# Optimization experiments

Measured on AMD Instinct MI355X. Metric: run time of the kernel, lower is better.

Reference implementation:

```python
import jax, jax.numpy as jnp
import numpy as np

B, T, D, H, E, S, K = 2, 2048, 768, 1536, 8, 1, 2
STD = 0.02


def setup_inputs() -> dict:
    key = jax.random.key(0)
    ks = jax.random.split(key, 8)
    x = jax.random.normal(ks[0], (B, T, D), jnp.float32)
    router_w = jax.random.normal(ks[1], (E, D), jnp.float32) * STD
    sw1 = jax.random.normal(ks[2], (S, D, H), jnp.float32) * STD
    sw2 = jax.random.normal(ks[3], (S, D, H), jnp.float32) * STD
    sproj = jax.random.normal(ks[4], (S, H, D), jnp.float32) * STD
    ew1 = jax.random.normal(ks[5], (E, D, H), jnp.float32) * STD
    ew2 = jax.random.normal(ks[6], (E, D, H), jnp.float32) * STD
    eproj = jax.random.normal(ks[7], (E, H, D), jnp.float32) * STD
    return {"x": x, "router_w": router_w, "sw1": sw1, "sw2": sw2,
            "sproj": sproj, "ew1": ew1, "ew2": ew2, "eproj": eproj,
            "top_k": K}


def reference(x, router_w, sw1, sw2, sproj, ew1, ew2, eproj, top_k):
    n_experts = router_w.shape[0]
    # Shared experts (SwiGLU), summed over the shared-expert axis s.
    a = jnp.einsum('btd,sdh->bsth', x, sw1)
    b = jnp.einsum('btd,sdh->bsth', x, sw2)
    shared_out = jnp.einsum('bsth,shd->btd', jax.nn.silu(a) * b, sproj)  # [B,T,D]

    # Router: note the original applies softmax and calls the result `logits`,
    # returning it as the second output.
    probs = jax.nn.softmax(jnp.einsum('btd,ed->bte', x, router_w), axis=-1)  # [B,T,E]
    top_vals, top_idx = jax.lax.top_k(probs, top_k)
    weights = top_vals / jnp.sum(top_vals, axis=-1, keepdims=True)  # renormalized [B,T,K]

    # Dense combine weights: combine[b,t,e] = sum_k weights[b,t,k] * 1[top_idx[b,t,k]==e]
    combine = jnp.sum(jax.nn.one_hot(top_idx, n_experts, dtype=x.dtype)
                      * weights[..., None], axis=-2)  # [B,T,E]

    # Routed experts: compute every expert densely, then mask/weight by combine.
    ea = jnp.einsum('btd,edh->bteh', x, ew1)
    eb = jnp.einsum('btd,edh->bteh', x, ew2)
    routed = jnp.einsum('bteh,ehd,bte->btd', jax.nn.silu(ea) * eb, eproj, combine)

    return shared_out + routed, probs
```

## Files before the change

### kernel.cpp

```cpp
#include <hip/hip_runtime.h>

typedef unsigned short u16;
typedef __bf16 bf16x8 __attribute__((ext_vector_type(8)));
typedef float f32x4 __attribute__((ext_vector_type(4)));

__device__ __forceinline__ u16 f2bf(float f) {
  union { float f; unsigned u; } v; v.f = f;
  return (u16)((v.u + 0x7fffu + ((v.u >> 16) & 1u)) >> 16);
}

#define GLDS16(g, l)                                                          \
  __builtin_amdgcn_global_load_lds(                                           \
      (const __attribute__((address_space(1))) void*)(g),                     \
      (__attribute__((address_space(3))) void*)(l), 16, 0, 0)

#define SBAR()  __builtin_amdgcn_s_barrier()
#define SCHED() __builtin_amdgcn_sched_barrier(0)
#define VMCNT(n) asm volatile("s_waitcnt vmcnt(" #n ")" ::: "memory")

#define NTOK 4096
#define DIM  768
#define HID  1536
#define NEXP 8
#define SLAB 1536
#define CAPR (NEXP * SLAB)
#define SHB  CAPR
#define NSLOT (CAPR + NTOK)
#define MAXT1 64
#define MAXT2 128
#define CSTRIDE 32

__global__ __launch_bounds__(256) void k_prep(const float* __restrict__ x,
                                              const float* __restrict__ rw,
                                              const float* __restrict__ ew1,
                                              const float* __restrict__ sw1,
                                              const float* __restrict__ ew2,
                                              const float* __restrict__ sw2,
                                              const float* __restrict__ eproj,
                                              const float* __restrict__ sproj,
                                              u16* __restrict__ dstBase,
                                              u16* __restrict__ xb,
                                              float* __restrict__ probs,
                                              int* __restrict__ cnt,
                                              int* __restrict__ slotTok,
                                              float* __restrict__ slotW,
                                              int* __restrict__ tokSlot) {
  constexpr size_t SL = (size_t)HID * DIM;
  const int z = blockIdx.z;
  if (z < 27) {
    __shared__ u16 tile[64][65];
    const float* src;
    int R, C, bxx = blockIdx.x, byy = blockIdx.y;
    if (z < 9)       { src = (z < 8) ? ew1 + (size_t)z * SL : sw1; R = DIM; C = HID; }
    else if (z < 18) { const int q = z - 9;  src = (q < 8) ? ew2 + (size_t)q * SL : sw2; R = DIM; C = HID; }
    else             { const int q = z - 18; src = (q < 8) ? eproj + (size_t)q * SL : sproj;
                       R = HID; C = DIM; const int t = bxx; bxx = byy; byy = t; }
    u16* dst = dstBase + (size_t)z * SL;
    const int c0 = bxx * 64, r0 = byy * 64;
    const int tx = threadIdx.x, ty = threadIdx.y;
    #pragma unroll
    for (int i = 0; i < 16; i++)
      tile[ty + 4 * i][tx] = f2bf(src[(size_t)(r0 + ty + 4 * i) * C + c0 + tx]);
    __syncthreads();
    #pragma unroll
    for (int i = 0; i < 16; i++)
      dst[(size_t)(c0 + ty + 4 * i) * R + r0 + tx] = tile[tx][ty + 4 * i];
    return;
  }
  __shared__ int   sI1[16], sI2[16];
  __shared__ float sW1[16], sW2[16];
  const int tid = threadIdx.y * 64 + threadIdx.x;
  const int wv = tid >> 6, lane = tid & 63;
  const int rb = blockIdx.y * 24 + blockIdx.x;
  for (int j = wv; j < 15; j += 4) {
    const int t = rb + 288 * j;
    if (t >= NTOK) continue;
    const float* xr = x + (size_t)t * DIM;
    u16* xbr = xb + (size_t)t * DIM;
    float acc[NEXP] = {0, 0, 0, 0, 0, 0, 0, 0};
    #pragma unroll
    for (int i = 0; i < DIM / 64; i++) {
      const int d = lane + 64 * i;
      const float xv = xr[d];
      xbr[d] = f2bf(xv);
      #pragma unroll
      for (int e = 0; e < NEXP; e++) acc[e] += xv * rw[e * DIM + d];
    }
    #pragma unroll
    for (int e = 0; e < NEXP; e++)
      #pragma unroll
      for (int s = 32; s > 0; s >>= 1) acc[e] += __shfl_xor(acc[e], s, 64);
    if (lane == 0) {
      float mx = acc[0];
      #pragma unroll
      for (int e = 1; e < NEXP; e++) mx = fmaxf(mx, acc[e]);
      float p[NEXP], sum = 0.f;
      #pragma unroll
      for (int e = 0; e < NEXP; e++) { p[e] = expf(acc[e] - mx); sum += p[e]; }
      const float inv = 1.f / sum;
      #pragma unroll
      for (int e = 0; e < NEXP; e++) p[e] *= inv;
      #pragma unroll
      for (int e = 0; e < NEXP; e++) probs[(size_t)t * NEXP + e] = p[e];
      int i1 = 0;
      #pragma unroll
      for (int e = 1; e < NEXP; e++) if (p[e] > p[i1]) i1 = e;
      int i2 = (i1 == 0) ? 1 : 0;
      #pragma unroll
      for (int e = 0; e < NEXP; e++) if (e != i1 && p[e] > p[i2]) i2 = e;
      const float s2 = 1.f / (p[i1] + p[i2]);
      sI1[j] = i1; sI2[j] = i2;
      sW1[j] = p[i1] * s2; sW2[j] = p[i2] * s2;
      slotTok[SHB + t] = t; slotW[SHB + t] = 1.f;
    }
  }
  __syncthreads();
  if (tid < NEXP) {
    const int e = tid;
    int c = 0;
    for (int j = 0; j < 15; j++) {
      const int t = rb + 288 * j;
      if (t < NTOK && (sI1[j] == e || sI2[j] == e)) c++;
    }
    if (c) {
      const int base = atomicAdd(&cnt[e * CSTRIDE], c);
      if (base + c <= SLAB) {
        int k = 0;
        for (int j = 0; j < 15; j++) {
          const int t = rb + 288 * j;
          if (t >= NTOK) continue;
          if (sI1[j] == e) {
            const int s = e * SLAB + base + k;
            slotTok[s] = t; slotW[s] = sW1[j]; tokSlot[2 * t] = s; k++;
          } else if (sI2[j] == e) {
            const int s = e * SLAB + base + k;
            slotTok[s] = t; slotW[s] = sW2[j]; tokSlot[2 * t + 1] = s; k++;
          }
        }
      }
    }
  }
}

__device__ __forceinline__ int decode_tile(const int* __restrict__ cnt, int bx,
                                           int rows_log2, int nShared, int* m0out) {
  int e = -1, m0 = 0, acc = 0;
  #pragma unroll
  for (int ee = 0; ee < NEXP; ee++) {
    const int tl = (cnt[ee * CSTRIDE] + ((1 << rows_log2) - 1)) >> rows_log2;
    if (bx >= acc && bx < acc + tl) { e = ee; m0 = ee * SLAB + ((bx - acc) << rows_log2); }
    acc += tl;
  }
  if (e < 0) {
    const int sx = bx - acc;
    if (sx >= 0 && sx < nShared) { e = NEXP; m0 = SHB + (sx << rows_log2); }
  }
  *m0out = m0;
  return e;
}

__global__ __launch_bounds__(512, 2) void k_gemm1(const u16* __restrict__ xb,
                                                  const u16* __restrict__ w1t,
                                                  const u16* __restrict__ w2t,
                                                  const int* __restrict__ cnt,
                                                  const int* __restrict__ slotTok,
                                                  const float* __restrict__ slotW,
                                                  u16* __restrict__ hidden) {
  __shared__ alignas(16) u16 L[2][32768];
  const int bid = blockIdx.x;
  const int wgid = (bid & 7) * 96 + (bid >> 3);
  const int bx = wgid % MAXT1, by = wgid / MAXT1;
  int m0;
  const int e = decode_tile(cnt, bx, 8, NTOK / 256, &m0);
  if (e < 0) return;
  const int nBase = by * 128;
  constexpr size_t SL = (size_t)HID * DIM;
  const u16* w1 = w1t + (size_t)e * SL;
  const u16* w2 = w2t + (size_t)e * SL;
  const int tid = threadIdx.x, w = tid >> 6, lane = tid & 63;
  const int wr = w >> 1, wc = w & 1;

  const int srow = tid >> 2;
  const int kcol = ((tid & 3) ^ ((tid >> 3) & 3)) * 8;
  const int tokA0 = slotTok[m0 + srow];
  const int tokA1 = slotTok[m0 + 128 + srow];
  const u16* gA0 = xb + (size_t)tokA0 * DIM + kcol;
  const u16* gA1 = xb + (size_t)tokA1 * DIM + kcol;
  const u16* gB1 = w1 + (size_t)(nBase + srow) * DIM + kcol;
  const u16* gB2 = w2 + (size_t)(nBase + srow) * DIM + kcol;
  const int dA0 = tid * 8, dA1 = 4096 + tid * 8, dB = tid * 8;

  const int rl = lane & 15;
  const int kq = lane >> 4;
  const int aBase = (wr * 64 + rl) * 32 + (kq ^ ((rl >> 1) & 3)) * 8;
  const int bBase = (wc * 64 + rl) * 32 + (kq ^ ((rl >> 1) & 3)) * 8;

  f32x4 acc1[4][4], acc2[4][4];
  const f32x4 vz = {0.f, 0.f, 0.f, 0.f};
  #pragma unroll
  for (int m = 0; m < 4; m++)
    #pragma unroll
    for (int n = 0; n < 4; n++) { acc1[m][n] = vz; acc2[m][n] = vz; }

#define G1_STKH(d, koff, kh) do {                                             \
    GLDS16(gA0 + (koff), &L[d][(kh) * 8192 + dA0]);                           \
    GLDS16(gA1 + (koff), &L[d][(kh) * 8192 + dA1]);                           \
    GLDS16(gB1 + (koff), &L[d][16384 + (kh) * 4096 + dB]);                    \
    GLDS16(gB2 + (koff), &L[d][24576 + (kh) * 4096 + dB]); } while (0)

#define G1_PH(d, kh, dostage, sd, skh, koff, vm) do {                         \
    bf16x8 av[4], b1v[4], b2v[4];                                             \
    _Pragma("unroll")                                                         \
    for (int n = 0; n < 4; n++) {                                             \
      b1v[n] = *(const bf16x8*)&L[d][16384 + (kh) * 4096 + bBase + n * 512];  \
      b2v[n] = *(const bf16x8*)&L[d][24576 + (kh) * 4096 + bBase + n * 512];  \
    }                                                                         \
    _Pragma("unroll")                                                         \
    for (int m = 0; m < 4; m++)                                               \
      av[m] = *(const bf16x8*)&L[d][(kh) * 8192 + aBase + m * 512];           \
    SCHED();                                                                  \
    if (dostage) { G1_STKH(sd, koff, skh); SCHED(); }                         \
    __builtin_amdgcn_s_setprio(1);                                            \
    _Pragma("unroll")                                                         \
    for (int m = 0; m < 4; m++)                                               \
      _Pragma("unroll")                                                       \
      for (int n = 0; n < 4; n++) {                                           \
        acc1[m][n] = __builtin_amdgcn_mfma_f32_16x16x32_bf16(av[m], b1v[n], acc1[m][n], 0, 0, 0); \
        acc2[m][n] = __builtin_amdgcn_mfma_f32_16x16x32_bf16(av[m], b2v[n], acc2[m][n], 0, 0, 0); \
      }                                                                       \
    __builtin_amdgcn_s_setprio(0);                                            \
    SCHED(); VMCNT(vm); SBAR(); SCHED();                                      \
  } while (0)

  G1_STKH(0, 0, 0);
  G1_STKH(0, 32, 1);
  G1_STKH(1, 64, 0);
  SCHED(); VMCNT(8); SBAR(); SCHED();

  for (int i = 0; i < 5; i++) {
    const int kt = i * 128;
    G1_PH(0, 0, true, 1, 1, kt + 96,  8);
    G1_PH(0, 1, true, 0, 0, kt + 128, 8);
    G1_PH(1, 0, true, 0, 1, kt + 160, 8);
    G1_PH(1, 1, true, 1, 0, kt + 192, 8);
  }
  G1_PH(0, 0, true, 1, 1, 736, 8);
  G1_PH(0, 1, false, 0, 0, 0, 4);
  G1_PH(1, 0, false, 0, 0, 0, 0);
  G1_PH(1, 1, false, 0, 0, 0, 0);
#undef G1_PH
#undef G1_STKH

  #pragma unroll
  for (int m = 0; m < 4; m++)
    #pragma unroll
    for (int r = 0; r < 4; r++) {
      const int slot = m0 + wr * 64 + m * 16 + (lane >> 4) * 4 + r;
      const float cwv = slotW[slot];
      #pragma unroll
      for (int n = 0; n < 4; n++) {
        const int hcol = nBase + wc * 64 + n * 16 + (lane & 15);
        const float v1 = acc1[m][n][r], v2 = acc2[m][n][r];
        hidden[(size_t)slot * HID + hcol] = f2bf((v1 / (1.f + __expf(-v1))) * v2 * cwv);
      }
    }
}

__global__ __launch_bounds__(256, 2) void k_gemm2(const u16* __restrict__ hid,
                                                  const u16* __restrict__ pjt,
                                                  const int* __restrict__ cnt,
                                                  float* __restrict__ g2) {
  __shared__ alignas(16) u16 L[2][16384];
  const int bid = blockIdx.x;
  const int wgid = (bid & 7) * 96 + (bid >> 3);
  const int bx = wgid % MAXT2, by = wgid / MAXT2;
  int m0;
  const int e = decode_tile(cnt, bx, 7, NTOK / 128, &m0);
  if (e < 0) return;
  const int nBase = by * 128;
  constexpr size_t SL = (size_t)HID * DIM;
  const u16* pj = pjt + (size_t)e * SL;
  const int tid = threadIdx.x, w = tid >> 6, lane = tid & 63;
  const int wr = w >> 1, wc = w & 1;

  const int r0 = tid >> 2;
  const int kcol = ((tid & 3) ^ ((tid >> 3) & 3)) * 8;
  const u16* gA0 = hid + (size_t)(m0 + r0) * HID + kcol;
  const u16* gA1 = hid + (size_t)(m0 + 64 + r0) * HID + kcol;
  const u16* gB0 = pj + (size_t)(nBase + r0) * HID + kcol;
  const u16* gB1p = pj + (size_t)(nBase + 64 + r0) * HID + kcol;
  const int d0 = tid * 8, d1 = 2048 + tid * 8;

  const int rl = lane & 15;
  const int kq = lane >> 4;
  const int aBase = (wr * 64 + rl) * 32 + (kq ^ ((rl >> 1) & 3)) * 8;
  const int bBase = (wc * 64 + rl) * 32 + (kq ^ ((rl >> 1) & 3)) * 8;

  f32x4 acc[4][4];
  const f32x4 vz = {0.f, 0.f, 0.f, 0.f};
  #pragma unroll
  for (int m = 0; m < 4; m++)
    #pragma unroll
    for (int n = 0; n < 4; n++) acc[m][n] = vz;

#define G2_STKH(d, koff, kh) do {                                             \
    GLDS16(gA0 + (koff), &L[d][(kh) * 4096 + d0]);                            \
    GLDS16(gA1 + (koff), &L[d][(kh) * 4096 + d1]);                            \
    GLDS16(gB0 + (koff), &L[d][8192 + (kh) * 4096 + d0]);                     \
    GLDS16(gB1p + (koff), &L[d][8192 + (kh) * 4096 + d1]); } while (0)

#define G2_PH(d, kh, dostage, sd, skh, koff, vm) do {                         \
    bf16x8 av[4], bv[4];                                                      \
    _Pragma("unroll")                                                         \
    for (int n = 0; n < 4; n++)                                               \
      bv[n] = *(const bf16x8*)&L[d][8192 + (kh) * 4096 + bBase + n * 512];    \
    _Pragma("unroll")                                                         \
    for (int m = 0; m < 4; m++)                                               \
      av[m] = *(const bf16x8*)&L[d][(kh) * 4096 + aBase + m * 512];           \
    SCHED();                                                                  \
    if (dostage) { G2_STKH(sd, koff, skh); SCHED(); }                         \
    __builtin_amdgcn_s_setprio(1);                                            \
    _Pragma("unroll")                                                         \
    for (int m = 0; m < 4; m++)                                               \
      _Pragma("unroll")                                                       \
      for (int n = 0; n < 4; n++)                                             \
        acc[m][n] = __builtin_amdgcn_mfma_f32_16x16x32_bf16(av[m], bv[n], acc[m][n], 0, 0, 0); \
    __builtin_amdgcn_s_setprio(0);                                            \
    SCHED(); VMCNT(vm); SBAR(); SCHED();                                      \
  } while (0)

  G2_STKH(0, 0, 0);
  G2_STKH(0, 32, 1);
  G2_STKH(1, 64, 0);
  SCHED(); VMCNT(8); SBAR(); SCHED();

  for (int i = 0; i < 11; i++) {
    const int kt = i * 128;
    G2_PH(0, 0, true, 1, 1, kt + 96,  8);
    G2_PH(0, 1, true, 0, 0, kt + 128, 8);
    G2_PH(1, 0, true, 0, 1, kt + 160, 8);
    G2_PH(1, 1, true, 1, 0, kt + 192, 8);
  }
  G2_PH(0, 0, true, 1, 1, 1504, 8);
  G2_PH(0, 1, false, 0, 0, 0, 4);
  G2_PH(1, 0, false, 0, 0, 0, 0);
  G2_PH(1, 1, false, 0, 0, 0, 0);
#undef G2_PH
#undef G2_STKH

  #pragma unroll
  for (int m = 0; m < 4; m++)
    #pragma unroll
    for (int r = 0; r < 4; r++) {
      const int slot = m0 + wr * 64 + m * 16 + (lane >> 4) * 4 + r;
      #pragma unroll
      for (int n = 0; n < 4; n++) {
        const int dcol = nBase + wc * 64 + n * 16 + (lane & 15);
        g2[(size_t)slot * DIM + dcol] = acc[m][n][r];
      }
    }
}

__global__ __launch_bounds__(192) void k_combine(const float* __restrict__ g2,
                                                 const int* __restrict__ tokSlot,
                                                 float* __restrict__ out) {
  const int t = blockIdx.x, d4 = threadIdx.x;
  const int sA = tokSlot[2 * t], sB = tokSlot[2 * t + 1];
  const float4 a = ((const float4*)(g2 + (size_t)sA * DIM))[d4];
  const float4 b = ((const float4*)(g2 + (size_t)sB * DIM))[d4];
  const float4 c = ((const float4*)(g2 + (size_t)(SHB + t) * DIM))[d4];
  float4 o;
  o.x = a.x + b.x + c.x; o.y = a.y + b.y + c.y;
  o.z = a.z + b.z + c.z; o.w = a.w + b.w + c.w;
  ((float4*)(out + (size_t)t * DIM))[d4] = o;
}

extern "C" void kernel_launch(void* const* d_in, const int* in_sizes, int n_in,
                              void* d_out, int out_size, void* d_ws, size_t ws_size,
                              hipStream_t stream) {
  const float* x     = (const float*)d_in[0];
  const float* rw    = (const float*)d_in[1];
  const float* sw1   = (const float*)d_in[2];
  const float* sw2   = (const float*)d_in[3];
  const float* sproj = (const float*)d_in[4];
  const float* ew1   = (const float*)d_in[5];
  const float* ew2   = (const float*)d_in[6];
  const float* eproj = (const float*)d_in[7];
  float* out   = (float*)d_out;
  float* probs = out + (size_t)NTOK * DIM;

  constexpr size_t SL = (size_t)HID * DIM;
  constexpr size_t off_xb   = 0;
  constexpr size_t off_w1t  = 6291456;
  constexpr size_t off_w2t  = off_w1t + 2 * 9 * SL;
  constexpr size_t off_pjt  = off_w2t + 2 * 9 * SL;
  constexpr size_t off_hid  = off_pjt + 2 * 9 * SL;
  constexpr size_t off_g2   = off_hid + (size_t)NSLOT * HID * 2;
  constexpr size_t off_meta = off_g2 + (size_t)NSLOT * DIM * 4;

  char* ws = (char*)d_ws;
  u16*   xb   = (u16*)(ws + off_xb);
  u16*   w1t  = (u16*)(ws + off_w1t);
  u16*   w2t  = (u16*)(ws + off_w2t);
  u16*   pjt  = (u16*)(ws + off_pjt);
  u16*   hid  = (u16*)(ws + off_hid);
  float* g2   = (float*)(ws + off_g2);
  char*  meta = ws + off_meta;
  int*   cnt     = (int*)meta;
  int*   slotTok = (int*)(meta + 1024);
  float* slotW   = (float*)(meta + 1024 + 65536);
  int*   tokSlot = (int*)(meta + 1024 + 131072);

  hipMemsetAsync(meta, 0, 1024 + 131072 + 32768, stream);

  k_prep<<<dim3(HID / 64, DIM / 64, 28), dim3(64, 4), 0, stream>>>(
      x, rw, ew1, sw1, ew2, sw2, eproj, sproj, w1t, xb,
      probs, cnt, slotTok, slotW, tokSlot);

  k_gemm1<<<MAXT1 * (HID / 128), 512, 0, stream>>>(xb, w1t, w2t, cnt,
                                                   slotTok, slotW, hid);
  k_gemm2<<<MAXT2 * (DIM / 128), 256, 0, stream>>>(hid, pjt, cnt, g2);
  k_combine<<<NTOK, 192, 0, stream>>>(g2, tokSlot, out);
}
```

Before: 195.2 us.

## Interleave w1/w2 weights into one concatenated matrix and retile gate GEMM to 128x128

The prep kernel now writes the gate and up projection weights into a single interleaved matrix, with 16-column groups alternating between w1 and w2, so one GEMM produces both halves. gemm1 changes from 512-thread 256x128 tiles with two accumulator sets to 256-thread 128x128 tiles with one accumulator set over the doubled N dimension, and applies SwiGLU by pairing adjacent n-fragments. The aim is lower register and LDS pressure and more blocks for occupancy and load balance. The cost is that each A tile is reloaded for twice as many N tiles, and the epilogue writes are narrower.

```diff
diff --git a/kernel.cpp b/kernel.cpp
--- a/kernel.cpp
+++ b/kernel.cpp
@@ -26,9 +26,9 @@
 #define CAPR (NEXP * SLAB)
 #define SHB  CAPR
 #define NSLOT (CAPR + NTOK)
-#define MAXT1 64
 #define MAXT2 128
 #define CSTRIDE 32
+
 
 __global__ __launch_bounds__(256) void k_prep(const float* __restrict__ x,
                                               const float* __restrict__ rw,
@@ -38,7 +38,8 @@
                                               const float* __restrict__ sw2,
                                               const float* __restrict__ eproj,
                                               const float* __restrict__ sproj,
-                                              u16* __restrict__ dstBase,
+                                              u16* __restrict__ bcat,
+                                              u16* __restrict__ pjt,
                                               u16* __restrict__ xb,
                                               float* __restrict__ probs,
                                               int* __restrict__ cnt,
@@ -49,22 +50,37 @@
   const int z = blockIdx.z;
   if (z < 27) {
     __shared__ u16 tile[64][65];
-    const float* src;
-    int R, C, bxx = blockIdx.x, byy = blockIdx.y;
-    if (z < 9)       { src = (z < 8) ? ew1 + (size_t)z * SL : sw1; R = DIM; C = HID; }
-    else if (z < 18) { const int q = z - 9;  src = (q < 8) ? ew2 + (size_t)q * SL : sw2; R = DIM; C = HID; }
-    else             { const int q = z - 18; src = (q < 8) ? eproj + (size_t)q * SL : sproj;
-                       R = HID; C = DIM; const int t = bxx; bxx = byy; byy = t; }
-    u16* dst = dstBase + (size_t)z * SL;
-    const int c0 = bxx * 64, r0 = byy * 64;
     const int tx = threadIdx.x, ty = threadIdx.y;
-    #pragma unroll
-    for (int i = 0; i < 16; i++)
-      tile[ty + 4 * i][tx] = f2bf(src[(size_t)(r0 + ty + 4 * i) * C + c0 + tx]);
-    __syncthreads();
-    #pragma unroll
-    for (int i = 0; i < 16; i++)
-      dst[(size_t)(c0 + ty + 4 * i) * R + r0 + tx] = tile[tx][ty + 4 * i];
+    if (z < 18) {
+      const int mat = (z >= 9) ? 1 : 0;
+      const int q = (z >= 9) ? z - 9 : z;
+      const float* src = (q < 8) ? ((mat == 0) ? ew1 + (size_t)q * SL : ew2 + (size_t)q * SL)
+                                 : ((mat == 0) ? sw1 : sw2);
+      u16* dst = bcat + (size_t)q * (2 * SL);
+      const int c0 = blockIdx.x * 64, r0 = blockIdx.y * 64;
+      #pragma unroll
+      for (int i = 0; i < 16; i++)
+        tile[ty + 4 * i][tx] = f2bf(src[(size_t)(r0 + ty + 4 * i) * HID + c0 + tx]);
+      __syncthreads();
+      #pragma unroll
+      for (int i = 0; i < 16; i++) {
+        const int c = c0 + ty + 4 * i;
+        const int ncat = ((c >> 4) << 5) + mat * 16 + (c & 15);
+        dst[(size_t)ncat * DIM + r0 + tx] = tile[tx][ty + 4 * i];
+      }
+    } else {
+      const int q = z - 18;
+      const float* src = (q < 8) ? eproj + (size_t)q * SL : sproj;
+      u16* dst = pjt + (size_t)q * SL;
+      const int c0 = blockIdx.y * 64, r0 = blockIdx.x * 64;
+      #pragma unroll
+      for (int i = 0; i < 16; i++)
+        tile[ty + 4 * i][tx] = f2bf(src[(size_t)(r0 + ty + 4 * i) * DIM + c0 + tx]);
+      __syncthreads();
+      #pragma unroll
+      for (int i = 0; i < 16; i++)
+        dst[(size_t)(c0 + ty + 4 * i) * HID + r0 + tx] = tile[tx][ty + 4 * i];
+    }
     return;
   }
   __shared__ int   sI1[16], sI2[16];
@@ -159,75 +175,69 @@
   return e;
 }
 
-__global__ __launch_bounds__(512, 2) void k_gemm1(const u16* __restrict__ xb,
-                                                  const u16* __restrict__ w1t,
-                                                  const u16* __restrict__ w2t,
+__global__ __launch_bounds__(256, 2) void k_gemm1(const u16* __restrict__ xb,
+                                                  const u16* __restrict__ bcat,
                                                   const int* __restrict__ cnt,
                                                   const int* __restrict__ slotTok,
                                                   const float* __restrict__ slotW,
                                                   u16* __restrict__ hidden) {
-  __shared__ alignas(16) u16 L[2][32768];
+  __shared__ alignas(16) u16 L[2][16384];
   const int bid = blockIdx.x;
-  const int wgid = (bid & 7) * 96 + (bid >> 3);
-  const int bx = wgid % MAXT1, by = wgid / MAXT1;
+  const int wgid = (bid & 7) * 384 + (bid >> 3);
+  const int bx = wgid % MAXT2, by = wgid / MAXT2;
   int m0;
-  const int e = decode_tile(cnt, bx, 8, NTOK / 256, &m0);
+  const int e = decode_tile(cnt, bx, 7, NTOK / 128, &m0);
   if (e < 0) return;
   const int nBase = by * 128;
   constexpr size_t SL = (size_t)HID * DIM;
-  const u16* w1 = w1t + (size_t)e * SL;
-  const u16* w2 = w2t + (size_t)e * SL;
+  const u16* bc = bcat + (size_t)e * (2 * SL);
   const int tid = threadIdx.x, w = tid >> 6, lane = tid & 63;
   const int wr = w >> 1, wc = w & 1;
 
-  const int srow = tid >> 2;
+  const int r0 = tid >> 2;
   const int kcol = ((tid & 3) ^ ((tid >> 3) & 3)) * 8;
-  const int tokA0 = slotTok[m0 + srow];
-  const int tokA1 = slotTok[m0 + 128 + srow];
+  const int tokA0 = slotTok[m0 + r0];
+  const int tokA1 = slotTok[m0 + 64 + r0];
   const u16* gA0 = xb + (size_t)tokA0 * DIM + kcol;
   const u16* gA1 = xb + (size_t)tokA1 * DIM + kcol;
-  const u16* gB1 = w1 + (size_t)(nBase + srow) * DIM + kcol;
-  const u16* gB2 = w2 + (size_t)(nBase + srow) * DIM + kcol;
-  const int dA0 = tid * 8, dA1 = 4096 + tid * 8, dB = tid * 8;
+  const u16* gB0 = bc + (size_t)(nBase + r0) * DIM + kcol;
+  const u16* gB1p = bc + (size_t)(nBase + 64 + r0) * DIM + kcol;
+  const int d0 = tid * 8, d1 = 2048 + tid * 8;
 
   const int rl = lane & 15;
   const int kq = lane >> 4;
   const int aBase = (wr * 64 + rl) * 32 + (kq ^ ((rl >> 1) & 3)) * 8;
   const int bBase = (wc * 64 + rl) * 32 + (kq ^ ((rl >> 1) & 3)) * 8;
 
-  f32x4 acc1[4][4], acc2[4][4];
+  f32x4 acc[4][4];
   const f32x4 vz = {0.f, 0.f, 0.f, 0.f};
   #pragma unroll
   for (int m = 0; m < 4; m++)
     #pragma unroll
-    for (int n = 0; n < 4; n++) { acc1[m][n] = vz; acc2[m][n] = vz; }
+    for (int n = 0; n < 4; n++) acc[m][n] = vz;
 
 #define G1_STKH(d, koff, kh) do {                                             \
-    GLDS16(gA0 + (koff), &L[d][(kh) * 8192 + dA0]);                           \
-    GLDS16(gA1 + (koff), &L[d][(kh) * 8192 + dA1]);                           \
-    GLDS16(gB1 + (koff), &L[d][16384 + (kh) * 4096 + dB]);                    \
-    GLDS16(gB2 + (koff), &L[d][24576 + (kh) * 4096 + dB]); } while (0)
+    GLDS16(gA0 + (koff), &L[d][(kh) * 4096 + d0]);                            \
+    GLDS16(gA1 + (koff), &L[d][(kh) * 4096 + d1]);                            \
+    GLDS16(gB0 + (koff), &L[d][8192 + (kh) * 4096 + d0]);                     \
+    GLDS16(gB1p + (koff), &L[d][8192 + (kh) * 4096 + d1]); } while (0)
 
 #define G1_PH(d, kh, dostage, sd, skh, koff, vm) do {                         \
-    bf16x8 av[4], b1v[4], b2v[4];                                             \
-    _Pragma("unroll")                                                         \
-    for (int n = 0; n < 4; n++) {                                             \
-      b1v[n] = *(const bf16x8*)&L[d][16384 + (kh) * 4096 + bBase + n * 512];  \
-      b2v[n] = *(const bf16x8*)&L[d][24576 + (kh) * 4096 + bBase + n * 512];  \
-    }                                                                         \
+    bf16x8 av[4], bv[4];                                                      \
+    _Pragma("unroll")                                                         \
+    for (int n = 0; n < 4; n++)                                               \
+      bv[n] = *(const bf16x8*)&L[d][8192 + (kh) * 4096 + bBase + n * 512];    \
     _Pragma("unroll")                                                         \
     for (int m = 0; m < 4; m++)                                               \
-      av[m] = *(const bf16x8*)&L[d][(kh) * 8192 + aBase + m * 512];           \
+      av[m] = *(const bf16x8*)&L[d][(kh) * 4096 + aBase + m * 512];           \
     SCHED();                                                                  \
     if (dostage) { G1_STKH(sd, koff, skh); SCHED(); }                         \
     __builtin_amdgcn_s_setprio(1);                                            \
     _Pragma("unroll")                                                         \
     for (int m = 0; m < 4; m++)                                               \
       _Pragma("unroll")                                                       \
-      for (int n = 0; n < 4; n++) {                                           \
-        acc1[m][n] = __builtin_amdgcn_mfma_f32_16x16x32_bf16(av[m], b1v[n], acc1[m][n], 0, 0, 0); \
-        acc2[m][n] = __builtin_amdgcn_mfma_f32_16x16x32_bf16(av[m], b2v[n], acc2[m][n], 0, 0, 0); \
-      }                                                                       \
+      for (int n = 0; n < 4; n++)                                             \
+        acc[m][n] = __builtin_amdgcn_mfma_f32_16x16x32_bf16(av[m], bv[n], acc[m][n], 0, 0, 0); \
     __builtin_amdgcn_s_setprio(0);                                            \
     SCHED(); VMCNT(vm); SBAR(); SCHED();                                      \
   } while (0)
@@ -251,6 +261,7 @@
 #undef G1_PH
 #undef G1_STKH
 
+  const int hc0 = ((nBase + wc * 64) >> 1) + rl;
   #pragma unroll
   for (int m = 0; m < 4; m++)
     #pragma unroll
@@ -258,10 +269,10 @@
       const int slot = m0 + wr * 64 + m * 16 + (lane >> 4) * 4 + r;
       const float cwv = slotW[slot];
       #pragma unroll
-      for (int n = 0; n < 4; n++) {
-        const int hcol = nBase + wc * 64 + n * 16 + (lane & 15);
-        const float v1 = acc1[m][n][r], v2 = acc2[m][n][r];
-        hidden[(size_t)slot * HID + hcol] = f2bf((v1 / (1.f + __expf(-v1))) * v2 * cwv);
+      for (int p = 0; p < 2; p++) {
+        const float v1 = acc[m][2 * p][r], v2 = acc[m][2 * p + 1][r];
+        hidden[(size_t)slot * HID + hc0 + p * 16] =
+            f2bf((v1 / (1.f + __expf(-v1))) * v2 * cwv);
       }
     }
 }
@@ -391,17 +402,15 @@
 
   constexpr size_t SL = (size_t)HID * DIM;
   constexpr size_t off_xb   = 0;
-  constexpr size_t off_w1t  = 6291456;
-  constexpr size_t off_w2t  = off_w1t + 2 * 9 * SL;
-  constexpr size_t off_pjt  = off_w2t + 2 * 9 * SL;
+  constexpr size_t off_bcat = 6291456;
+  constexpr size_t off_pjt  = off_bcat + 2 * 2 * 9 * SL / 2 * 2;
   constexpr size_t off_hid  = off_pjt + 2 * 9 * SL;
   constexpr size_t off_g2   = off_hid + (size_t)NSLOT * HID * 2;
   constexpr size_t off_meta = off_g2 + (size_t)NSLOT * DIM * 4;
 
   char* ws = (char*)d_ws;
   u16*   xb   = (u16*)(ws + off_xb);
-  u16*   w1t  = (u16*)(ws + off_w1t);
-  u16*   w2t  = (u16*)(ws + off_w2t);
+  u16*   bcat = (u16*)(ws + off_bcat);
   u16*   pjt  = (u16*)(ws + off_pjt);
   u16*   hid  = (u16*)(ws + off_hid);
   float* g2   = (float*)(ws + off_g2);
@@ -414,11 +423,11 @@
   hipMemsetAsync(meta, 0, 1024 + 131072 + 32768, stream);
 
   k_prep<<<dim3(HID / 64, DIM / 64, 28), dim3(64, 4), 0, stream>>>(
-      x, rw, ew1, sw1, ew2, sw2, eproj, sproj, w1t, xb,
+      x, rw, ew1, sw1, ew2, sw2, eproj, sproj, bcat, pjt, xb,
       probs, cnt, slotTok, slotW, tokSlot);
 
-  k_gemm1<<<MAXT1 * (HID / 128), 512, 0, stream>>>(xb, w1t, w2t, cnt,
-                                                   slotTok, slotW, hid);
+  k_gemm1<<<MAXT2 * (2 * HID / 128), 256, 0, stream>>>(xb, bcat, cnt,
+                                                       slotTok, slotW, hid);
   k_gemm2<<<MAXT2 * (DIM / 128), 256, 0, stream>>>(hid, pjt, cnt, g2);
   k_combine<<<NTOK, 192, 0, stream>>>(g2, tokSlot, out);
 }
```

New measurement: 206.2 us. 5.7% more time.
